# Performance work log

Measured on AMD Instinct MI355X. Metric: run time of the kernel, lower is better.

## Reference

```python
import jax, jax.numpy as jnp
import numpy as np

B, S, D, H = 8, 2048, 768, 768

def setup_inputs() -> dict:
    key = jax.random.key(0)
    ks = jax.random.split(key, 8)
    s = 1.0 / np.sqrt(D)
    return {
        "x": jax.random.normal(ks[0], (B, S, D), dtype=jnp.float32),
        "y": jax.random.normal(ks[1], (B, S, D), dtype=jnp.float32),
        "Wq": jax.random.uniform(ks[2], (D, H), jnp.float32, -s, s),
        "bq": jax.random.uniform(ks[3], (H,), jnp.float32, -s, s),
        "Wk": jax.random.uniform(ks[4], (D, H), jnp.float32, -s, s),
        "bk": jax.random.uniform(ks[5], (H,), jnp.float32, -s, s),
        "Wv": jax.random.uniform(ks[6], (D, H), jnp.float32, -s, s),
        "bv": jax.random.uniform(ks[7], (H,), jnp.float32, -s, s),
    }

def reference(x, y, Wq, bq, Wk, bk, Wv, bv):
    q = jnp.einsum('bsd,dh->bsh', x, Wq) + bq      # [B,S,H]
    k = jnp.einsum('bsd,dh->bsh', x, Wk) + bk      # [B,S,H]
    v = jnp.einsum('bsd,dh->bsh', y, Wv) + bv      # [B,S,H]
    scores = jnp.einsum('bqh,bkh->bqk', q, k)      # [B,S,S], no scaling in original
    probs = jax.nn.softmax(scores, axis=-1)
    bilinear_v = q * v                              # elementwise gate
    context = jnp.einsum('bqk,bkh->bqh', probs, bilinear_v)
    return context  # dropout is identity in eval mode
```

## Files before the change

### kernel.cpp

```cpp
#include <hip/hip_runtime.h>
#include <cstdint>
#include <cstddef>


#define BM 128
#define BN 128
#define BK 32

using half8 = __attribute__((ext_vector_type(8))) _Float16;
using half4 = __attribute__((ext_vector_type(4))) _Float16;
using f32x4 = __attribute__((ext_vector_type(4))) float;

__global__ __launch_bounds__(256) void cvt2_f32_f16(
    const float* __restrict__ a, const float* __restrict__ b,
    _Float16* __restrict__ oa, _Float16* __restrict__ ob, int n4) {
  const float* in = blockIdx.y ? b : a;
  _Float16* out = blockIdx.y ? ob : oa;
  int i = blockIdx.x * 256 + threadIdx.x;
  if (i >= n4) return;
  float4 v = ((const float4*)in)[i];
  half4 o = {(_Float16)v.x, (_Float16)v.y, (_Float16)v.z, (_Float16)v.w};
  *(half4*)&out[(size_t)i * 4] = o;
}

__global__ __launch_bounds__(256) void tr3_cvt768(
    const float* __restrict__ Wq, const float* __restrict__ Wk,
    const float* __restrict__ Wv, _Float16* __restrict__ Wt) {
  const float* W = (blockIdx.y == 0) ? Wq : (blockIdx.y == 1) ? Wk : Wv;
  _Float16* o = Wt + (size_t)blockIdx.y * 589824;
  int i = blockIdx.x * 256 + threadIdx.x;
  int h = i / 768, d = i - h * 768;
  o[i] = (_Float16)W[d * 768 + h];
}

template <int MODE>
__global__ __launch_bounds__(256) void gemm_bt(
    const _Float16* __restrict__ Ab, int ldA, long sA,
    const _Float16* __restrict__ Bb, int ldB, long sB,
    void* __restrict__ Cb, int ldc, long sC,
    int K, const float* __restrict__ bias, const _Float16* __restrict__ qb,
    const float* __restrict__ bias2, void* __restrict__ Cb2) {
  __shared__ __align__(16) _Float16 lA[BM * BK];
  __shared__ __align__(16) _Float16 lB[BN * BK];

  const int tid  = threadIdx.x;
  const int lane = tid & 63;
  const int quad = lane >> 4;
  const int l15  = lane & 15;
  const int wave = tid >> 6;
  const int wm = (wave >> 1) * 64;
  const int wn = (wave & 1) * 64;
  const long bm = (long)blockIdx.x * BM;
  const long bn = (long)blockIdx.y * BN;
  const _Float16* A = Ab + (long)blockIdx.z * sA;
  const _Float16* B = Bb + (long)blockIdx.z * sB;

  f32x4 acc[4][4] = {};

  const int c0 = tid,        r0 = c0 >> 2, k0c = (c0 & 3) * 8;
  const int c1 = 256 + tid,  r1 = c1 >> 2, k1c = (c1 & 3) * 8;
  const _Float16* gA0 = A + (size_t)(bm + r0) * ldA + k0c;
  const _Float16* gA1 = A + (size_t)(bm + r1) * ldA + k1c;
  const _Float16* gB0 = B + (size_t)(bn + r0) * ldB + k0c;
  const _Float16* gB1 = B + (size_t)(bn + r1) * ldB + k1c;

  for (int kk = 0; kk < K; kk += BK) {
    __syncthreads();
    __builtin_amdgcn_global_load_lds(
        (const __attribute__((address_space(1))) void*)(gA0 + kk),
        (__attribute__((address_space(3))) void*)&lA[c0 * 8], 16, 0, 0);
    __builtin_amdgcn_global_load_lds(
        (const __attribute__((address_space(1))) void*)(gA1 + kk),
        (__attribute__((address_space(3))) void*)&lA[c1 * 8], 16, 0, 0);
    __builtin_amdgcn_global_load_lds(
        (const __attribute__((address_space(1))) void*)(gB0 + kk),
        (__attribute__((address_space(3))) void*)&lB[c0 * 8], 16, 0, 0);
    __builtin_amdgcn_global_load_lds(
        (const __attribute__((address_space(1))) void*)(gB1 + kk),
        (__attribute__((address_space(3))) void*)&lB[c1 * 8], 16, 0, 0);
    __syncthreads();

    half8 af[4], bfr[4];
#pragma unroll
    for (int i = 0; i < 4; i++) {
      af[i]  = *(const half8*)&lA[(wm + i * 16 + l15) * BK + quad * 8];
      bfr[i] = *(const half8*)&lB[(wn + i * 16 + l15) * BK + quad * 8];
    }
#pragma unroll
    for (int i = 0; i < 4; i++)
#pragma unroll
      for (int j = 0; j < 4; j++)
        acc[i][j] = __builtin_amdgcn_mfma_f32_16x16x32_f16(
            af[i], bfr[j], acc[i][j], 0, 0, 0);
  }

  if constexpr (MODE == 1) {
    __shared__ __align__(16) _Float16 xp[4 * 32 * 72];
    _Float16* xw = &xp[wave * 2304];
    const long sbase = (bm & 2047) + wm;
    const long bb = bm >> 11;
    const long hbase = bn + wn;
#pragma unroll
    for (int jh = 0; jh < 2; jh++) {
      __syncthreads();
#pragma unroll
      for (int j2 = 0; j2 < 2; j2++) {
        const int j = jh * 2 + j2;
        const long n_g = hbase + j * 16 + l15;
        const float bsv = bias[n_g];
#pragma unroll
        for (int i = 0; i < 4; i++) {
          half4 pk;
#pragma unroll
          for (int r = 0; r < 4; r++) {
            long m_g = bm + wm + i * 16 + quad * 4 + r;
            float v = acc[i][j][r] + bsv;
            float q = (float)qb[m_g * (long)ldc + n_g];
            pk[r] = (_Float16)(v * q);
          }
          *(half4*)&xw[(j2 * 16 + l15) * 72 + i * 16 + quad * 4] = pk;
        }
      }
      __syncthreads();
#pragma unroll
      for (int t = 0; t < 4; t++) {
        const int n_r = t * 8 + (lane >> 3);
        const int m8 = (lane & 7) * 8;
        half8 vv = *(const half8*)&xw[n_r * 72 + m8];
        *(half8*)&((_Float16*)Cb)[(bb * 768 + hbase + 32 * jh + n_r) * 2048 +
                                  sbase + m8] = vv;
      }
    }
  } else {
#pragma unroll
    for (int i = 0; i < 4; i++) {
#pragma unroll
      for (int j = 0; j < 4; j++) {
#pragma unroll
        for (int r = 0; r < 4; r++) {
          long m = bm + wm + i * 16 + quad * 4 + r;
          long n = bn + wn + j * 16 + l15;
          float v = acc[i][j][r];
          if constexpr (MODE == 3) {
            const bool isq = (bn < 768);
            long nn = isq ? n : n - 768;
            v += (isq ? bias : bias2)[nn];
            _Float16* dst = (_Float16*)(isq ? Cb : Cb2);
            dst[m * ldc + nn] = (_Float16)v;
          } else {
            ((float*)Cb + (long)blockIdx.z * sC)[m * ldc + n] = v;
          }
        }
      }
    }
  }
}

__global__ __launch_bounds__(256) void softmax_rows(
    const float* __restrict__ sc, _Float16* __restrict__ pr, int prPitch) {
  const int row = blockIdx.x;
  const float* x = sc + (size_t)row * 2048;
  const int t = threadIdx.x;
  float4 v0 = ((const float4*)x)[2 * t];
  float4 v1 = ((const float4*)x)[2 * t + 1];
  float e[8] = {v0.x, v0.y, v0.z, v0.w, v1.x, v1.y, v1.z, v1.w};

  float m = e[0];
#pragma unroll
  for (int i = 1; i < 8; i++) m = fmaxf(m, e[i]);
#pragma unroll
  for (int o = 32; o; o >>= 1) m = fmaxf(m, __shfl_xor(m, o, 64));
  __shared__ float red[4];
  if ((t & 63) == 0) red[t >> 6] = m;
  __syncthreads();
  m = fmaxf(fmaxf(red[0], red[1]), fmaxf(red[2], red[3]));

  float s = 0.f;
#pragma unroll
  for (int i = 0; i < 8; i++) { e[i] = __expf(e[i] - m); s += e[i]; }
#pragma unroll
  for (int o = 32; o; o >>= 1) s += __shfl_xor(s, o, 64);
  __syncthreads();
  if ((t & 63) == 0) red[t >> 6] = s;
  __syncthreads();
  s = red[0] + red[1] + red[2] + red[3];
  float inv = 1.0f / s;

  union { _Float16 h[8]; uint4 v; } o;
#pragma unroll
  for (int i = 0; i < 8; i++) o.h[i] = (_Float16)(e[i] * inv);
  ((uint4*)(pr + (size_t)row * prPitch))[t] = o.v;
}

extern "C" void kernel_launch(void* const* d_in, const int* in_sizes, int n_in,
                              void* d_out, int out_size, void* d_ws, size_t ws_size,
                              hipStream_t stream) {
  const float* x  = (const float*)d_in[0];
  const float* y  = (const float*)d_in[1];
  const float* Wq = (const float*)d_in[2];
  const float* bq = (const float*)d_in[3];
  const float* Wk = (const float*)d_in[4];
  const float* bk = (const float*)d_in[5];
  const float* Wv = (const float*)d_in[6];
  const float* bv = (const float*)d_in[7];
  float* out = (float*)d_out;

  const int S = 2048, D = 768, H = 768;
  const long SH = (long)S * H;
  char* ws = (char*)d_ws;
  _Float16* qb  = (_Float16*)(ws + 0);
  _Float16* kb  = (_Float16*)(ws + 25165824);
  _Float16* gT  = (_Float16*)(ws + 50331648);
  _Float16* xb  = (_Float16*)(ws + 75497472);
  _Float16* yb  = (_Float16*)(ws + 100663296);
  _Float16* WtQ = (_Float16*)(ws + 125829120);
  _Float16* WtV = WtQ + 2 * 589824;
  float* scores = (float*)(ws + 75497472);

  cvt2_f32_f16<<<dim3(12288, 2), 256, 0, stream>>>(x, y, xb, yb, 3145728);
  tr3_cvt768<<<dim3(2304, 3), 256, 0, stream>>>(Wq, Wk, Wv, WtQ);

  gemm_bt<3><<<dim3(128, 12, 1), 256, 0, stream>>>(
      xb, D, 0, WtQ, D, 0, qb, H, 0, D, bq, nullptr, bk, kb);
  gemm_bt<1><<<dim3(128, 6, 1), 256, 0, stream>>>(
      yb, D, 0, WtV, D, 0, gT, H, 0, D, bv, qb, nullptr, nullptr);

  _Float16* probs = (_Float16*)scores;
  if (ws_size >= 209715200ull) {
    gemm_bt<2><<<dim3(16, 16, 8), 256, 0, stream>>>(
        qb, H, SH, kb, H, SH, scores, S, (long)S * S, H,
        nullptr, nullptr, nullptr, nullptr);
    softmax_rows<<<16384, 256, 0, stream>>>(scores, probs, 4096);
    gemm_bt<2><<<dim3(16, 6, 8), 256, 0, stream>>>(
        probs, 4096, (long)S * 4096, gT, S, SH, out, H, SH, S,
        nullptr, nullptr, nullptr, nullptr);
  } else {
    for (int r = 0; r < 4; r++) {
      const long b0 = 2 * r;
      gemm_bt<2><<<dim3(16, 16, 2), 256, 0, stream>>>(
          qb + b0 * SH, H, SH, kb + b0 * SH, H, SH, scores, S, (long)S * S, H,
          nullptr, nullptr, nullptr, nullptr);
      softmax_rows<<<4096, 256, 0, stream>>>(scores, probs, 4096);
      gemm_bt<2><<<dim3(16, 6, 2), 256, 0, stream>>>(
          probs, 4096, (long)S * 4096, gT + b0 * SH, S, SH,
          out + b0 * SH, H, SH, S, nullptr, nullptr, nullptr, nullptr);
    }
  }
}
```

Baseline: 449.4 us.

## Fuse fp32-to-fp16 conversion into GEMMs and softmax into score/PV GEMMs

Removes the separate x/y fp32-to-fp16 conversion kernel; the projection GEMMs now load fp32 activations and convert them into LDS. Removes the softmax kernel: the score GEMM atomically accumulates per-row sums of exp(score), and the PV GEMM reads fp32 scores and applies exp and 1/sum while staging them into LDS. There is no max subtraction, which risks overflow for large scores. The change trades kernel launches and an fp16 probs write/read for fp32 score reads and extra exp work inside the GEMM.

```diff
diff --git a/kernel.cpp b/kernel.cpp
--- a/kernel.cpp
+++ b/kernel.cpp
@@ -8,24 +8,17 @@
 #define BK 32
 
 using half8 = __attribute__((ext_vector_type(8))) _Float16;
-using half4 = __attribute__((ext_vector_type(4))) _Float16;
 using f32x4 = __attribute__((ext_vector_type(4))) float;
-
-__global__ __launch_bounds__(256) void cvt2_f32_f16(
-    const float* __restrict__ a, const float* __restrict__ b,
-    _Float16* __restrict__ oa, _Float16* __restrict__ ob, int n4) {
-  const float* in = blockIdx.y ? b : a;
-  _Float16* out = blockIdx.y ? ob : oa;
-  int i = blockIdx.x * 256 + threadIdx.x;
-  if (i >= n4) return;
-  float4 v = ((const float4*)in)[i];
-  half4 o = {(_Float16)v.x, (_Float16)v.y, (_Float16)v.z, (_Float16)v.w};
-  *(half4*)&out[(size_t)i * 4] = o;
-}
 
 __global__ __launch_bounds__(256) void tr3_cvt768(
     const float* __restrict__ Wq, const float* __restrict__ Wk,
-    const float* __restrict__ Wv, _Float16* __restrict__ Wt) {
+    const float* __restrict__ Wv, _Float16* __restrict__ Wt,
+    float* __restrict__ lz, int nz) {
+  if (blockIdx.y == 3) {
+    int i = blockIdx.x * 256 + threadIdx.x;
+    if (i < nz) lz[i] = 0.0f;
+    return;
+  }
   const float* W = (blockIdx.y == 0) ? Wq : (blockIdx.y == 1) ? Wk : Wv;
   _Float16* o = Wt + (size_t)blockIdx.y * 589824;
   int i = blockIdx.x * 256 + threadIdx.x;
@@ -33,13 +26,14 @@
   o[i] = (_Float16)W[d * 768 + h];
 }
 
-template <int MODE>
+template <int MODE, int ASRC>
 __global__ __launch_bounds__(256) void gemm_bt(
-    const _Float16* __restrict__ Ab, int ldA, long sA,
+    const void* __restrict__ Ab, int ldA, long sA,
     const _Float16* __restrict__ Bb, int ldB, long sB,
     void* __restrict__ Cb, int ldc, long sC,
-    int K, const float* __restrict__ bias, const _Float16* __restrict__ qb,
-    const float* __restrict__ bias2, void* __restrict__ Cb2) {
+    int K, const float* __restrict__ bias, const _Float16* __restrict__ qg,
+    const float* __restrict__ bias2, void* __restrict__ Cb2,
+    float* __restrict__ lsum) {
   __shared__ __align__(16) _Float16 lA[BM * BK];
   __shared__ __align__(16) _Float16 lB[BN * BK];
 
@@ -52,32 +46,77 @@
   const int wn = (wave & 1) * 64;
   const long bm = (long)blockIdx.x * BM;
   const long bn = (long)blockIdx.y * BN;
-  const _Float16* A = Ab + (long)blockIdx.z * sA;
-  const _Float16* B = Bb + (long)blockIdx.z * sB;
 
   f32x4 acc[4][4] = {};
 
   const int c0 = tid,        r0 = c0 >> 2, k0c = (c0 & 3) * 8;
   const int c1 = 256 + tid,  r1 = c1 >> 2, k1c = (c1 & 3) * 8;
-  const _Float16* gA0 = A + (size_t)(bm + r0) * ldA + k0c;
-  const _Float16* gA1 = A + (size_t)(bm + r1) * ldA + k1c;
+
+  const _Float16* B = Bb + (long)blockIdx.z * sB;
   const _Float16* gB0 = B + (size_t)(bn + r0) * ldB + k0c;
   const _Float16* gB1 = B + (size_t)(bn + r1) * ldB + k1c;
 
+  const _Float16* gA0 = nullptr; const _Float16* gA1 = nullptr;
+  const float* fA0 = nullptr; const float* fA1 = nullptr;
+  float invl0 = 0.f, invl1 = 0.f;
+  if constexpr (ASRC == 0) {
+    const _Float16* A = (const _Float16*)Ab + (long)blockIdx.z * sA;
+    gA0 = A + (size_t)(bm + r0) * ldA + k0c;
+    gA1 = A + (size_t)(bm + r1) * ldA + k1c;
+  } else {
+    const float* Af = (const float*)Ab + (long)blockIdx.z * sA;
+    fA0 = Af + (size_t)(bm + r0) * ldA + k0c;
+    fA1 = Af + (size_t)(bm + r1) * ldA + k1c;
+    if constexpr (ASRC == 2) {
+      const float* lr = lsum + (long)blockIdx.z * 2048 + bm;
+      invl0 = 1.0f / lr[r0];
+      invl1 = 1.0f / lr[r1];
+    }
+  }
+
   for (int kk = 0; kk < K; kk += BK) {
     __syncthreads();
-    __builtin_amdgcn_global_load_lds(
-        (const __attribute__((address_space(1))) void*)(gA0 + kk),
-        (__attribute__((address_space(3))) void*)&lA[c0 * 8], 16, 0, 0);
-    __builtin_amdgcn_global_load_lds(
-        (const __attribute__((address_space(1))) void*)(gA1 + kk),
-        (__attribute__((address_space(3))) void*)&lA[c1 * 8], 16, 0, 0);
+    float4 a00, a01, a10, a11;
+    if constexpr (ASRC != 0) {
+      a00 = *(const float4*)(fA0 + kk);
+      a01 = *(const float4*)(fA0 + kk + 4);
+      a10 = *(const float4*)(fA1 + kk);
+      a11 = *(const float4*)(fA1 + kk + 4);
+    } else {
+      __builtin_amdgcn_global_load_lds(
+          (const __attribute__((address_space(1))) void*)(gA0 + kk),
+          (__attribute__((address_space(3))) void*)&lA[c0 * 8], 16, 0, 0);
+      __builtin_amdgcn_global_load_lds(
+          (const __attribute__((address_space(1))) void*)(gA1 + kk),
+          (__attribute__((address_space(3))) void*)&lA[c1 * 8], 16, 0, 0);
+    }
     __builtin_amdgcn_global_load_lds(
         (const __attribute__((address_space(1))) void*)(gB0 + kk),
         (__attribute__((address_space(3))) void*)&lB[c0 * 8], 16, 0, 0);
     __builtin_amdgcn_global_load_lds(
         (const __attribute__((address_space(1))) void*)(gB1 + kk),
         (__attribute__((address_space(3))) void*)&lB[c1 * 8], 16, 0, 0);
+    if constexpr (ASRC == 1) {
+      half8 h0 = {(_Float16)a00.x, (_Float16)a00.y, (_Float16)a00.z,
+                  (_Float16)a00.w, (_Float16)a01.x, (_Float16)a01.y,
+                  (_Float16)a01.z, (_Float16)a01.w};
+      half8 h1 = {(_Float16)a10.x, (_Float16)a10.y, (_Float16)a10.z,
+                  (_Float16)a10.w, (_Float16)a11.x, (_Float16)a11.y,
+                  (_Float16)a11.z, (_Float16)a11.w};
+      *(half8*)&lA[c0 * 8] = h0;
+      *(half8*)&lA[c1 * 8] = h1;
+    } else if constexpr (ASRC == 2) {
+      half8 h0 = {(_Float16)(__expf(a00.x) * invl0), (_Float16)(__expf(a00.y) * invl0),
+                  (_Float16)(__expf(a00.z) * invl0), (_Float16)(__expf(a00.w) * invl0),
+                  (_Float16)(__expf(a01.x) * invl0), (_Float16)(__expf(a01.y) * invl0),
+                  (_Float16)(__expf(a01.z) * invl0), (_Float16)(__expf(a01.w) * invl0)};
+      half8 h1 = {(_Float16)(__expf(a10.x) * invl1), (_Float16)(__expf(a10.y) * invl1),
+                  (_Float16)(__expf(a10.z) * invl1), (_Float16)(__expf(a10.w) * invl1),
+                  (_Float16)(__expf(a11.x) * invl1), (_Float16)(__expf(a11.y) * invl1),
+                  (_Float16)(__expf(a11.z) * invl1), (_Float16)(__expf(a11.w) * invl1)};
+      *(half8*)&lA[c0 * 8] = h0;
+      *(half8*)&lA[c1 * 8] = h1;
+    }
     __syncthreads();
 
     half8 af[4], bfr[4];
@@ -100,6 +139,7 @@
     const long sbase = (bm & 2047) + wm;
     const long bb = bm >> 11;
     const long hbase = bn + wn;
+    using half4v = __attribute__((ext_vector_type(4))) _Float16;
 #pragma unroll
     for (int jh = 0; jh < 2; jh++) {
       __syncthreads();
@@ -110,15 +150,15 @@
         const float bsv = bias[n_g];
 #pragma unroll
         for (int i = 0; i < 4; i++) {
-          half4 pk;
+          half4v pk;
 #pragma unroll
           for (int r = 0; r < 4; r++) {
             long m_g = bm + wm + i * 16 + quad * 4 + r;
             float v = acc[i][j][r] + bsv;
-            float q = (float)qb[m_g * (long)ldc + n_g];
+            float q = (float)qg[m_g * (long)ldc + n_g];
             pk[r] = (_Float16)(v * q);
           }
-          *(half4*)&xw[(j2 * 16 + l15) * 72 + i * 16 + quad * 4] = pk;
+          *(half4v*)&xw[(j2 * 16 + l15) * 72 + i * 16 + quad * 4] = pk;
         }
       }
       __syncthreads();
@@ -131,65 +171,53 @@
                                   sbase + m8] = vv;
       }
     }
-  } else {
-#pragma unroll
-    for (int i = 0; i < 4; i++) {
-#pragma unroll
-      for (int j = 0; j < 4; j++) {
+  } else if constexpr (MODE == 3) {
+    const bool isq = (bn < 768);
+#pragma unroll
+    for (int i = 0; i < 4; i++)
+#pragma unroll
+      for (int j = 0; j < 4; j++)
 #pragma unroll
         for (int r = 0; r < 4; r++) {
           long m = bm + wm + i * 16 + quad * 4 + r;
           long n = bn + wn + j * 16 + l15;
+          long nn = isq ? n : n - 768;
+          float v = acc[i][j][r] + (isq ? bias : bias2)[nn];
+          ((_Float16*)(isq ? Cb : Cb2))[m * ldc + nn] = (_Float16)v;
+        }
+  } else if constexpr (MODE == 4) {
+    float* Cf = (float*)Cb + (long)blockIdx.z * sC;
+    float* lrow = lsum + (long)blockIdx.z * 2048 + bm + wm;
+#pragma unroll
+    for (int i = 0; i < 4; i++)
+#pragma unroll
+      for (int r = 0; r < 4; r++) {
+        float es = 0.f;
+#pragma unroll
+        for (int j = 0; j < 4; j++) {
+          long m = bm + wm + i * 16 + quad * 4 + r;
+          long n = bn + wn + j * 16 + l15;
           float v = acc[i][j][r];
-          if constexpr (MODE == 3) {
-            const bool isq = (bn < 768);
-            long nn = isq ? n : n - 768;
-            v += (isq ? bias : bias2)[nn];
-            _Float16* dst = (_Float16*)(isq ? Cb : Cb2);
-            dst[m * ldc + nn] = (_Float16)v;
-          } else {
-            ((float*)Cb + (long)blockIdx.z * sC)[m * ldc + n] = v;
-          }
-        }
+          Cf[m * ldc + n] = v;
+          es += __expf(v);
+        }
+#pragma unroll
+        for (int o = 1; o < 16; o <<= 1) es += __shfl_xor(es, o, 64);
+        if (l15 == 0) atomicAdd(&lrow[i * 16 + quad * 4 + r], es);
       }
-    }
-  }
-}
-
-__global__ __launch_bounds__(256) void softmax_rows(
-    const float* __restrict__ sc, _Float16* __restrict__ pr, int prPitch) {
-  const int row = blockIdx.x;
-  const float* x = sc + (size_t)row * 2048;
-  const int t = threadIdx.x;
-  float4 v0 = ((const float4*)x)[2 * t];
-  float4 v1 = ((const float4*)x)[2 * t + 1];
-  float e[8] = {v0.x, v0.y, v0.z, v0.w, v1.x, v1.y, v1.z, v1.w};
-
-  float m = e[0];
-#pragma unroll
-  for (int i = 1; i < 8; i++) m = fmaxf(m, e[i]);
-#pragma unroll
-  for (int o = 32; o; o >>= 1) m = fmaxf(m, __shfl_xor(m, o, 64));
-  __shared__ float red[4];
-  if ((t & 63) == 0) red[t >> 6] = m;
-  __syncthreads();
-  m = fmaxf(fmaxf(red[0], red[1]), fmaxf(red[2], red[3]));
-
-  float s = 0.f;
-#pragma unroll
-  for (int i = 0; i < 8; i++) { e[i] = __expf(e[i] - m); s += e[i]; }
-#pragma unroll
-  for (int o = 32; o; o >>= 1) s += __shfl_xor(s, o, 64);
-  __syncthreads();
-  if ((t & 63) == 0) red[t >> 6] = s;
-  __syncthreads();
-  s = red[0] + red[1] + red[2] + red[3];
-  float inv = 1.0f / s;
-
-  union { _Float16 h[8]; uint4 v; } o;
-#pragma unroll
-  for (int i = 0; i < 8; i++) o.h[i] = (_Float16)(e[i] * inv);
-  ((uint4*)(pr + (size_t)row * prPitch))[t] = o.v;
+  } else {
+    float* Cf = (float*)Cb + (long)blockIdx.z * sC;
+#pragma unroll
+    for (int i = 0; i < 4; i++)
+#pragma unroll
+      for (int j = 0; j < 4; j++)
+#pragma unroll
+        for (int r = 0; r < 4; r++) {
+          long m = bm + wm + i * 16 + quad * 4 + r;
+          long n = bn + wn + j * 16 + l15;
+          Cf[m * ldc + n] = acc[i][j][r];
+        }
+  }
 }
 
 extern "C" void kernel_launch(void* const* d_in, const int* in_sizes, int n_in,
@@ -207,43 +235,45 @@
 
   const int S = 2048, D = 768, H = 768;
   const long SH = (long)S * H;
+  const long SS = (long)S * S;
   char* ws = (char*)d_ws;
-  _Float16* qb  = (_Float16*)(ws + 0);
-  _Float16* kb  = (_Float16*)(ws + 25165824);
-  _Float16* gT  = (_Float16*)(ws + 50331648);
-  _Float16* xb  = (_Float16*)(ws + 75497472);
-  _Float16* yb  = (_Float16*)(ws + 100663296);
-  _Float16* WtQ = (_Float16*)(ws + 125829120);
-  _Float16* WtV = WtQ + 2 * 589824;
-  float* scores = (float*)(ws + 75497472);
-
-  cvt2_f32_f16<<<dim3(12288, 2), 256, 0, stream>>>(x, y, xb, yb, 3145728);
-  tr3_cvt768<<<dim3(2304, 3), 256, 0, stream>>>(Wq, Wk, Wv, WtQ);
-
-  gemm_bt<3><<<dim3(128, 12, 1), 256, 0, stream>>>(
-      xb, D, 0, WtQ, D, 0, qb, H, 0, D, bq, nullptr, bk, kb);
-  gemm_bt<1><<<dim3(128, 6, 1), 256, 0, stream>>>(
-      yb, D, 0, WtV, D, 0, gT, H, 0, D, bv, qb, nullptr, nullptr);
-
-  _Float16* probs = (_Float16*)scores;
-  if (ws_size >= 209715200ull) {
-    gemm_bt<2><<<dim3(16, 16, 8), 256, 0, stream>>>(
-        qb, H, SH, kb, H, SH, scores, S, (long)S * S, H,
-        nullptr, nullptr, nullptr, nullptr);
-    softmax_rows<<<16384, 256, 0, stream>>>(scores, probs, 4096);
-    gemm_bt<2><<<dim3(16, 6, 8), 256, 0, stream>>>(
-        probs, 4096, (long)S * 4096, gT, S, SH, out, H, SH, S,
-        nullptr, nullptr, nullptr, nullptr);
+  _Float16* qb = (_Float16*)(ws + 0);
+  _Float16* kb = (_Float16*)(ws + 25165824);
+  _Float16* gT = (_Float16*)(ws + 50331648);
+  _Float16* Wt = (_Float16*)(ws + 142737408);
+  _Float16* WtV = Wt + 2 * 589824;
+
+  const bool tierA = ws_size >= 209780736ull;
+  float* scoresA = (float*)(ws + 75497472);
+  float* lA_     = (float*)(ws + 209715200);
+  float* lB_     = (float*)(ws + 75497472);
+  float* scoresB = (float*)(ws + 75628544);
+
+  float* lz = tierA ? lA_ : lB_;
+  tr3_cvt768<<<dim3(2304, 4), 256, 0, stream>>>(Wq, Wk, Wv, Wt, lz, 16384);
+
+  gemm_bt<3, 1><<<dim3(128, 12, 1), 256, 0, stream>>>(
+      x, D, 0, Wt, D, 0, qb, H, 0, D, bq, nullptr, bk, kb, nullptr);
+  gemm_bt<1, 1><<<dim3(128, 6, 1), 256, 0, stream>>>(
+      y, D, 0, WtV, D, 0, gT, H, 0, D, bv, qb, nullptr, nullptr, nullptr);
+
+  if (tierA) {
+    gemm_bt<4, 0><<<dim3(16, 16, 8), 256, 0, stream>>>(
+        qb, H, SH, kb, H, SH, scoresA, S, SS, H,
+        nullptr, nullptr, nullptr, nullptr, lA_);
+    gemm_bt<5, 2><<<dim3(16, 6, 8), 256, 0, stream>>>(
+        scoresA, S, SS, gT, S, SH, out, H, SH, S,
+        nullptr, nullptr, nullptr, nullptr, lA_);
   } else {
-    for (int r = 0; r < 4; r++) {
-      const long b0 = 2 * r;
-      gemm_bt<2><<<dim3(16, 16, 2), 256, 0, stream>>>(
-          qb + b0 * SH, H, SH, kb + b0 * SH, H, SH, scores, S, (long)S * S, H,
-          nullptr, nullptr, nullptr, nullptr);
-      softmax_rows<<<4096, 256, 0, stream>>>(scores, probs, 4096);
-      gemm_bt<2><<<dim3(16, 6, 2), 256, 0, stream>>>(
-          probs, 4096, (long)S * 4096, gT + b0 * SH, S, SH,
-          out + b0 * SH, H, SH, S, nullptr, nullptr, nullptr, nullptr);
+    for (int r = 0; r < 2; r++) {
+      const long b0 = 4 * r;
+      float* lr_ = lB_ + r * 8192;
+      gemm_bt<4, 0><<<dim3(16, 16, 4), 256, 0, stream>>>(
+          qb + b0 * SH, H, SH, kb + b0 * SH, H, SH, scoresB, S, SS, H,
+          nullptr, nullptr, nullptr, nullptr, lr_);
+      gemm_bt<5, 2><<<dim3(16, 6, 4), 256, 0, stream>>>(
+          scoresB, S, SS, gT + b0 * SH, S, SH, out + b0 * S * H, H, SH, S,
+          nullptr, nullptr, nullptr, nullptr, lr_);
     }
   }
 }
```

Result: slower. 474.1 us (+5.5%).
